# Optimization experiments

Hardware: AMD Instinct MI355X
Metric: run time of the kernel (lower is better)

Reference implementation:

```python
import jax, jax.numpy as jnp
import numpy as np

G = 4  # number of groups


def _group_vals(h, shift, Ua, Ua1, Ua2, Ua3):
    # h: [B, H]; Ua: [g, H/g, r]; Ua1/2/3: [g, r, H/g]
    B, H = h.shape
    hg = h.reshape(B, G, H // G)
    if shift:
        # torch index = rotate-left by `shift`: new group j reads old group (j+shift)%g
        hg = jnp.roll(hg, -shift, axis=1)
    t = jnp.einsum('bgd,gdr->bgr', hg, Ua)  # shared low-rank projection
    proj = lambda M: jnp.einsum('bgr,grd->bgd', t, M).reshape(B, H)
    return proj(Ua1), proj(Ua2), proj(Ua3)


def setup_inputs() -> dict:
    key = jax.random.key(0)
    ks = jax.random.split(key, 24)
    B, I, H, wR = 8192, 1024, 1024, 256
    hg = H // G
    r01, r23 = 64, 32
    d = {}
    d['x'] = jax.random.normal(ks[0], (B, I), dtype=jnp.float32)
    d['h'] = jax.random.normal(ks[1], (B, H), dtype=jnp.float32)
    d['W'] = 0.1 * jax.random.normal(ks[2], (I, wR), dtype=jnp.float32)
    d['W1'] = 0.1 * jax.random.normal(ks[3], (wR, H), dtype=jnp.float32)
    d['W2'] = 0.1 * jax.random.normal(ks[4], (wR, H), dtype=jnp.float32)
    d['W3'] = 0.1 * jax.random.normal(ks[5], (wR, H), dtype=jnp.float32)
    d['U'] = 0.1 * jax.random.normal(ks[6], (G, hg, r01), dtype=jnp.float32)
    d['U1'] = 0.1 * jax.random.normal(ks[7], (G, r01, hg), dtype=jnp.float32)
    d['U2'] = 0.1 * jax.random.normal(ks[8], (G, r01, hg), dtype=jnp.float32)
    d['U3'] = 0.1 * jax.random.normal(ks[9], (G, r01, hg), dtype=jnp.float32)
    d['UU'] = 0.1 * jax.random.normal(ks[10], (G, hg, r01), dtype=jnp.float32)
    d['UU1'] = 0.1 * jax.random.normal(ks[11], (G, r01, hg), dtype=jnp.float32)
    d['UU2'] = 0.1 * jax.random.normal(ks[12], (G, r01, hg), dtype=jnp.float32)
    d['UU3'] = 0.1 * jax.random.normal(ks[13], (G, r01, hg), dtype=jnp.float32)
    d['UUU'] = 0.1 * jax.random.normal(ks[14], (G, hg, r23), dtype=jnp.float32)
    d['UUU1'] = 0.1 * jax.random.normal(ks[15], (G, r23, hg), dtype=jnp.float32)
    d['UUU2'] = 0.1 * jax.random.normal(ks[16], (G, r23, hg), dtype=jnp.float32)
    d['UUU3'] = 0.1 * jax.random.normal(ks[17], (G, r23, hg), dtype=jnp.float32)
    d['UUUU'] = 0.1 * jax.random.normal(ks[18], (G, hg, r23), dtype=jnp.float32)
    d['UUUU1'] = 0.1 * jax.random.normal(ks[19], (G, r23, hg), dtype=jnp.float32)
    d['UUUU2'] = 0.1 * jax.random.normal(ks[20], (G, r23, hg), dtype=jnp.float32)
    d['UUUU3'] = 0.1 * jax.random.normal(ks[21], (G, r23, hg), dtype=jnp.float32)
    d['bias_r'] = jnp.ones((1, H), dtype=jnp.float32)
    d['bias_gate'] = jnp.ones((1, H), dtype=jnp.float32)
    d['bias_update'] = jnp.ones((1, H), dtype=jnp.float32)
    return d


def reference(x, h, W, W1, W2, W3, U, U1, U2, U3, UU, UU1, UU2, UU3,
              UUU, UUU1, UUU2, UUU3, UUUU, UUUU1, UUUU2, UUUU3,
              bias_r, bias_gate, bias_update):
    u1, u2, u3 = _group_vals(h, 0, U, U1, U2, U3)
    uu1, uu2, uu3 = _group_vals(h, 1, UU, UU1, UU2, UU3)
    uuu1, uuu2, uuu3 = _group_vals(h, 2, UUU, UUU1, UUU2, UUU3)
    uuuu1, uuuu2, uuuu3 = _group_vals(h, 3, UUUU, UUUU1, UUUU2, UUUU3)
    xw = x @ W  # [B, wRank]
    w1, w2, w3 = xw @ W1, xw @ W2, xw @ W3
    r = jax.nn.sigmoid(w1 + u1 + uu1 + uuu1 + uuuu1 + bias_r)
    z = jax.nn.sigmoid(w2 + u2 + uu2 + uuu2 + uuuu2 + bias_gate)
    c_tilda = jnp.tanh(w3 + r * (u3 + uu3 + uuu3 + uuuu3) + bias_update)
    return z * h + (1.0 - z) * c_tilda
```

## Files before the change

kernel.cpp:

```cpp
#include <hip/hip_runtime.h>

typedef short bf16x8 __attribute__((ext_vector_type(8)));
typedef float f32x4 __attribute__((ext_vector_type(4)));

__device__ __forceinline__ unsigned short f2bf(float f) {
  union { float f; unsigned u; } c; c.f = f;
  unsigned u = c.u;
  u += 0x7FFFu + ((u >> 16) & 1u);
  return (unsigned short)(u >> 16);
}
__device__ __forceinline__ float bf2f(unsigned short h) {
  union { unsigned u; float f; } c; c.u = ((unsigned)h) << 16;
  return c.f;
}
__device__ __forceinline__ void split2(float v, unsigned short& hi, unsigned short& lo) {
  union { float f; unsigned u; } c; c.f = v;
  unsigned uh = c.u & 0xFFFF0000u;
  hi = (unsigned short)(uh >> 16);
  union { unsigned u; float f; } d; d.u = uh;
  lo = f2bf(v - d.f);
}
__device__ __forceinline__ void gload16(const void* g, void* l) {
  __builtin_amdgcn_global_load_lds((const __attribute__((address_space(1))) void*)g,
                                   (__attribute__((address_space(3))) void*)l, 16, 0, 0);
}
__device__ __forceinline__ float sigm(float x) { return 1.0f / (1.0f + __expf(-x)); }
__device__ __forceinline__ float tanha(float x) { return 1.0f - 2.0f / (1.0f + __expf(2.0f * x)); }

__global__ __launch_bounds__(256) void s123(
    const float* __restrict__ W,
    const float* __restrict__ U, const float* __restrict__ UU,
    const float* __restrict__ UUU, const float* __restrict__ UUUU,
    const float* __restrict__ W1, const float* __restrict__ W2, const float* __restrict__ W3,
    const float* __restrict__ A1, const float* __restrict__ A2, const float* __restrict__ A3,
    const float* __restrict__ B1, const float* __restrict__ B2, const float* __restrict__ B3,
    const float* __restrict__ C1, const float* __restrict__ C2, const float* __restrict__ C3,
    const float* __restrict__ D1, const float* __restrict__ D2, const float* __restrict__ D3,
    unsigned short* __restrict__ Wt, unsigned short* __restrict__ Bg,
    unsigned short* __restrict__ Btp) {
  int gidx = blockIdx.x * 256 + threadIdx.x;
  if (gidx < 262144) {
    int idx = gidx;
    int n = idx >> 10, k = idx & 1023;
    Wt[idx] = f2bf(W[k * 256 + n]);
  } else if (gidx < 458752) {
    int idx = gidx - 262144;
    int g = idx / 49152;
    int rem = idx - g * 49152;
    int n = rem >> 8, k = rem & 255;
    int jj = 0, rr = n;
#pragma unroll
    for (int s = 0; s < 3; ++s) {
      int w = (((g - jj) & 3) < 2) ? 64 : 32;
      if (rr >= w) { rr -= w; ++jj; }
    }
    int v = (g - jj) & 3;
    int rv = (v < 2) ? 64 : 32;
    const float* M = (v == 0) ? U : (v == 1) ? UU : (v == 2) ? UUU : UUUU;
    Bg[idx] = f2bf(M[(jj * 256 + k) * rv + rr]);
  } else {
    int idx = gidx - 458752;
    int j  = idx / 540672;
    int r1 = idx - j * 540672;
    int kt = r1 / 49152;
    int r2 = r1 - kt * 49152;
    int c2 = r2 / 3072;
    int r3 = r2 - c2 * 3072;
    int q  = r3 >> 10;
    int r4 = r3 & 1023;
    int c16 = r4 >> 6;
    int k2  = r4 & 63;
    int c = c2 * 16 + c16;
    float val;
    if (kt < 8) {
      int kk = (kt * 64 + k2) & 255;
      const float* Wp = (q == 0) ? W1 : (q == 1) ? W2 : W3;
      val = Wp[kk * 1024 + j * 256 + c];
    } else {
      int kT = (kt - 8) * 64 + k2;
      int v, r, rv;
      if (kT < 64)       { v = 0; r = kT;       rv = 64; }
      else if (kT < 128) { v = 1; r = kT - 64;  rv = 64; }
      else if (kT < 160) { v = 2; r = kT - 128; rv = 32; }
      else               { v = 3; r = kT - 160; rv = 32; }
      const float* M;
      if (v == 0)      M = (q == 0) ? A1 : (q == 1) ? A2 : A3;
      else if (v == 1) M = (q == 0) ? B1 : (q == 1) ? B2 : B3;
      else if (v == 2) M = (q == 0) ? C1 : (q == 1) ? C2 : C3;
      else             M = (q == 0) ? D1 : (q == 1) ? D2 : D3;
      val = M[(j * rv + r) * 256 + c];
    }
    Btp[idx] = f2bf(val);
  }
}

__global__ __launch_bounds__(256) void g1_xw(const float* __restrict__ x,
                                             const unsigned short* __restrict__ Wt,
                                             unsigned short* __restrict__ Abuf) {
  __shared__ char lds[49152];
  const int tid = threadIdx.x, lane = tid & 63, wid = tid >> 6;
  const int mb = blockIdx.x, nb = blockIdx.y;
  const int wn = wid;
  f32x4 acc[2][2] = {};
  float4 xr[2];
  const int r0 = tid >> 4, f4c = tid & 15;
  const float* xbase = x + (size_t)(mb * 32) * 1024 + f4c * 4;

  auto loadX = [&](int kt) {
#pragma unroll
    for (int q = 0; q < 2; ++q)
      xr[q] = *(const float4*)(xbase + (size_t)(q * 16 + r0) * 1024 + kt * 64);
  };
  auto writeA = [&](int buf) {
#pragma unroll
    for (int q = 0; q < 2; ++q) {
      int row = q * 16 + r0;
      float4 v = xr[q];
      unsigned short h0, h1, h2, h3, l0, l1, l2, l3;
      split2(v.x, h0, l0); split2(v.y, h1, l1);
      split2(v.z, h2, l2); split2(v.w, h3, l3);
      int ba = row * 128 + ((f4c * 8) ^ ((row & 7) << 4));
      *(uint2*)(lds + buf * 4096 + ba) =
          make_uint2(((unsigned)h1 << 16) | h0, ((unsigned)h3 << 16) | h2);
      *(uint2*)(lds + 8192 + buf * 4096 + ba) =
          make_uint2(((unsigned)l1 << 16) | l0, ((unsigned)l3 << 16) | l2);
    }
  };
  auto stageB = [&](int kt, int buf) {
#pragma unroll
    for (int it = 0; it < 4; ++it) {
      int nloc = it * 32 + wid * 8 + (lane >> 3);
      const char* src = (const char*)Wt + (size_t)(nb * 128 + nloc) * 2048 + kt * 128
                        + (((lane & 7) * 16) ^ ((nloc & 7) << 4));
      gload16(src, lds + 16384 + buf * 16384 + (it * 32 + wid * 8) * 128);
    }
  };

  loadX(0); stageB(0, 0); writeA(0);
  __syncthreads();
#pragma unroll 2
  for (int kt = 0; kt < 16; ++kt) {
    int buf = kt & 1;
    if (kt < 15) {
      loadX(kt + 1); stageB(kt + 1, buf ^ 1);
      asm volatile("s_waitcnt vmcnt(6)" ::: "memory");
    } else {
      asm volatile("s_waitcnt vmcnt(0)" ::: "memory");
    }
    __builtin_amdgcn_s_barrier();
    __builtin_amdgcn_sched_barrier(0);
    const char* hA = lds + buf * 4096;
    const char* lA = lds + 8192 + buf * 4096;
    const char* bB = lds + 16384 + buf * 16384;
#pragma unroll
    for (int ks = 0; ks < 2; ++ks) {
      bf16x8 ah[2], al[2], b[2];
#pragma unroll
      for (int mf = 0; mf < 2; ++mf) {
        int mloc = mf * 16 + (lane & 15);
        int ka = (ks * 64 + (lane >> 4) * 16) ^ ((mloc & 7) << 4);
        ah[mf] = *(const bf16x8*)(hA + mloc * 128 + ka);
        al[mf] = *(const bf16x8*)(lA + mloc * 128 + ka);
      }
#pragma unroll
      for (int nf = 0; nf < 2; ++nf) {
        int nloc = wn * 32 + nf * 16 + (lane & 15);
        int kb = (ks * 64 + (lane >> 4) * 16) ^ ((nloc & 7) << 4);
        b[nf] = *(const bf16x8*)(bB + nloc * 128 + kb);
      }
#pragma unroll
      for (int mf = 0; mf < 2; ++mf)
#pragma unroll
        for (int nf = 0; nf < 2; ++nf) {
          acc[mf][nf] = __builtin_amdgcn_mfma_f32_16x16x32_bf16(ah[mf], b[nf], acc[mf][nf], 0, 0, 0);
          acc[mf][nf] = __builtin_amdgcn_mfma_f32_16x16x32_bf16(al[mf], b[nf], acc[mf][nf], 0, 0, 0);
        }
    }
    if (kt < 15) writeA(buf ^ 1);
    __builtin_amdgcn_sched_barrier(0);
    asm volatile("s_waitcnt lgkmcnt(0)" ::: "memory");
    __builtin_amdgcn_s_barrier();
  }
#pragma unroll
  for (int mf = 0; mf < 2; ++mf)
#pragma unroll
    for (int nf = 0; nf < 2; ++nf)
#pragma unroll
      for (int r = 0; r < 4; ++r) {
        int row = mb * 32 + mf * 16 + (lane >> 4) * 4 + r;
        int col = nb * 128 + wn * 32 + nf * 16 + (lane & 15);
        float val = acc[mf][nf][r];
        unsigned short hi, lo;
        split2(val, hi, lo);
        Abuf[(size_t)row * 1280 + col] = hi;
        Abuf[(size_t)row * 1280 + 256 + col] = lo;
      }
}

__global__ __launch_bounds__(256) void g2_t(const float* __restrict__ h,
                                            const unsigned short* __restrict__ Bg,
                                            unsigned short* __restrict__ Abuf) {
  __shared__ char lds[65536];
  const int tid = threadIdx.x, lane = tid & 63, wid = tid >> 6;
  const int mb = blockIdx.x, g = blockIdx.y;
  const int wm = wid >> 1, wn = wid & 1;
  f32x4 acc[2][6] = {};
  float4 hr[4];
  const int r0 = tid >> 4, f4c = tid & 15;
  const float* hbase = h + (size_t)(mb * 64) * 1024 + g * 256 + f4c * 4;

  auto loadH = [&](int kt) {
#pragma unroll
    for (int q = 0; q < 4; ++q)
      hr[q] = *(const float4*)(hbase + (size_t)(q * 16 + r0) * 1024 + kt * 64);
  };
  auto writeA = [&](int buf) {
#pragma unroll
    for (int q = 0; q < 4; ++q) {
      int row = q * 16 + r0;
      float4 v = hr[q];
      int ba = row * 128 + ((f4c * 8) ^ ((row & 7) << 4));
      *(uint2*)(lds + buf * 8192 + ba) =
          make_uint2(((unsigned)f2bf(v.y) << 16) | f2bf(v.x),
                     ((unsigned)f2bf(v.w) << 16) | f2bf(v.z));
    }
  };
  auto stageB = [&](int kt, int buf) {
#pragma unroll
    for (int it = 0; it < 6; ++it) {
      int nloc = it * 32 + wid * 8 + (lane >> 3);
      const char* src = (const char*)Bg + (size_t)(g * 192 + nloc) * 512 + kt * 128
                        + (((lane & 7) * 16) ^ ((nloc & 7) << 4));
      gload16(src, lds + 16384 + buf * 24576 + (it * 32 + wid * 8) * 128);
    }
  };

  loadH(0); stageB(0, 0); writeA(0);
  __syncthreads();
#pragma unroll
  for (int kt = 0; kt < 4; ++kt) {
    int buf = kt & 1;
    if (kt < 3) { loadH(kt + 1); stageB(kt + 1, buf ^ 1); }
    const char* cA = lds + buf * 8192;
    const char* cB = lds + 16384 + buf * 24576;
#pragma unroll
    for (int ks = 0; ks < 2; ++ks) {
      bf16x8 a[2], b[6];
#pragma unroll
      for (int mf = 0; mf < 2; ++mf) {
        int mloc = wm * 32 + mf * 16 + (lane & 15);
        int ka = (ks * 64 + (lane >> 4) * 16) ^ ((mloc & 7) << 4);
        a[mf] = *(const bf16x8*)(cA + mloc * 128 + ka);
      }
#pragma unroll
      for (int nf = 0; nf < 6; ++nf) {
        int nloc = wn * 96 + nf * 16 + (lane & 15);
        int kb = (ks * 64 + (lane >> 4) * 16) ^ ((nloc & 7) << 4);
        b[nf] = *(const bf16x8*)(cB + nloc * 128 + kb);
      }
#pragma unroll
      for (int mf = 0; mf < 2; ++mf)
#pragma unroll
        for (int nf = 0; nf < 6; ++nf)
          acc[mf][nf] = __builtin_amdgcn_mfma_f32_16x16x32_bf16(a[mf], b[nf], acc[mf][nf], 0, 0, 0);
    }
    if (kt < 3) writeA(buf ^ 1);
    __syncthreads();
  }
#pragma unroll
  for (int mf = 0; mf < 2; ++mf)
#pragma unroll
    for (int nf = 0; nf < 6; ++nf) {
      int n = wn * 96 + nf * 16 + (lane & 15);
      int jj = 0, rr = n;
#pragma unroll
      for (int s = 0; s < 3; ++s) {
        int w = (((g - jj) & 3) < 2) ? 64 : 32;
        if (rr >= w) { rr -= w; ++jj; }
      }
      int v = (g - jj) & 3;
      int offv = (v < 2) ? (v << 6) : (64 + (v << 5));
      int col = 512 + jj * 192 + offv + rr;
#pragma unroll
      for (int r = 0; r < 4; ++r) {
        int row = mb * 64 + wm * 32 + mf * 16 + (lane >> 4) * 4 + r;
        Abuf[(size_t)row * 1280 + col] = f2bf(acc[mf][nf][r]);
      }
    }
}

__global__ __launch_bounds__(256) void g3_main(const unsigned short* __restrict__ Abuf,
                                               const unsigned short* __restrict__ Btp,
                                               const float* __restrict__ h,
                                               const float* __restrict__ bias_r,
                                               const float* __restrict__ bias_g,
                                               const float* __restrict__ bias_u,
                                               float* __restrict__ out) {
  __shared__ char lds[57344];
  const int tid = threadIdx.x, lane = tid & 63, wid = tid >> 6;
  const int mb = blockIdx.x, nb = blockIdx.y, j = blockIdx.z;
  const int wm = wid >> 1, wn = wid & 1;
  f32x4 acc[4][4] = {};

  const char* AbufB = (const char*)Abuf + (size_t)mb * 128 * 2560;
  const char* BtpJ  = (const char*)Btp + (size_t)j * 1081344;
  int thrA[4], dstA[4], thrB[3], dstB[3];
#pragma unroll
  for (int it = 0; it < 4; ++it) {
    int mloc = wid * 32 + it * 8 + (lane >> 3);
    thrA[it] = mloc * 2560 + (((lane & 7) * 16) ^ ((mloc & 7) << 4));
    dstA[it] = wid * 4096 + it * 1024;
  }
#pragma unroll
  for (int it = 0; it < 3; ++it) {
    int row = it * 32 + wid * 8 + (lane >> 3);
    thrB[it] = row * 128 + (((lane & 7) * 16) ^ ((row & 7) << 4));
    dstB[it] = (it * 32 + wid * 8) * 128;
  }
  const char* pA[4][2];
  const char* pB[3][2];
#pragma unroll
  for (int mf = 0; mf < 4; ++mf) {
    int mloc = wm * 64 + mf * 16 + (lane & 15);
#pragma unroll
    for (int ks = 0; ks < 2; ++ks)
      pA[mf][ks] = lds + mloc * 128 + ((ks * 64 + (lane >> 4) * 16) ^ ((mloc & 7) << 4));
  }
#pragma unroll
  for (int q = 0; q < 3; ++q) {
    int nloc = wn * 48 + q * 16 + (lane & 15);
#pragma unroll
    for (int ks = 0; ks < 2; ++ks)
      pB[q][ks] = lds + 32768 + nloc * 128 + ((ks * 64 + (lane >> 4) * 16) ^ ((nloc & 7) << 4));
  }

  auto stage = [&](int kt, int buf) {
    int colb2 = (kt < 8) ? kt * 128 : (1024 + j * 384 + (kt - 8) * 128);
#pragma unroll
    for (int it = 0; it < 4; ++it)
      gload16(AbufB + colb2 + thrA[it], lds + buf * 16384 + dstA[it]);
    const char* bsrc = BtpJ + (size_t)(kt * 16 + nb * 2) * 6144;
#pragma unroll
    for (int it = 0; it < 3; ++it)
      gload16(bsrc + thrB[it], lds + 32768 + buf * 12288 + dstB[it]);
  };

  stage(0, 0);
#pragma unroll
  for (int kt = 0; kt < 11; ++kt) {
    int buf = kt & 1;
    if (kt < 10) {
      stage(kt + 1, buf ^ 1);
      asm volatile("s_waitcnt vmcnt(7)" ::: "memory");
    } else {
      asm volatile("s_waitcnt vmcnt(0)" ::: "memory");
    }
    __builtin_amdgcn_s_barrier();
    __builtin_amdgcn_sched_barrier(0);
    __builtin_amdgcn_s_setprio(1);
#pragma unroll
    for (int ks = 0; ks < 2; ++ks) {
      bf16x8 a[4];
#pragma unroll
      for (int mf = 0; mf < 4; ++mf)
        a[mf] = *(const bf16x8*)(pA[mf][ks] + buf * 16384);
#pragma unroll
      for (int q = 0; q < 3; ++q) {
        int p = (kt < 8) ? q : ((q == 2) ? 3 : q);
        bf16x8 b = *(const bf16x8*)(pB[q][ks] + buf * 12288);
#pragma unroll
        for (int mf = 0; mf < 4; ++mf)
          acc[mf][p] = __builtin_amdgcn_mfma_f32_16x16x32_bf16(a[mf], b, acc[mf][p], 0, 0, 0);
      }
    }
    __builtin_amdgcn_s_setprio(0);
    __builtin_amdgcn_sched_barrier(0);
    asm volatile("s_waitcnt lgkmcnt(0)" ::: "memory");
    __builtin_amdgcn_s_barrier();
  }
  int cg = j * 256 + nb * 32 + wn * 16 + (lane & 15);
  float br = bias_r[cg], bg = bias_g[cg], bu = bias_u[cg];
#pragma unroll
  for (int mf = 0; mf < 4; ++mf)
#pragma unroll
    for (int r = 0; r < 4; ++r) {
      int row = mb * 128 + wm * 64 + mf * 16 + (lane >> 4) * 4 + r;
      float p0 = acc[mf][0][r], p1 = acc[mf][1][r];
      float p2 = acc[mf][2][r], p3 = acc[mf][3][r];
      float rr = sigm(p0 + br);
      float zz = sigm(p1 + bg);
      float ct = tanha(p2 + rr * p3 + bu);
      float hv = h[(size_t)row * 1024 + cg];
      out[(size_t)row * 1024 + cg] = zz * hv + (1.0f - zz) * ct;
    }
}

extern "C" void kernel_launch(void* const* d_in, const int* in_sizes, int n_in,
                              void* d_out, int out_size, void* d_ws, size_t ws_size,
                              hipStream_t stream) {
  const float* x   = (const float*)d_in[0];
  const float* h   = (const float*)d_in[1];
  const float* W   = (const float*)d_in[2];
  const float* W1  = (const float*)d_in[3];
  const float* W2  = (const float*)d_in[4];
  const float* W3  = (const float*)d_in[5];
  const float* U   = (const float*)d_in[6];
  const float* U1  = (const float*)d_in[7];
  const float* U2  = (const float*)d_in[8];
  const float* U3  = (const float*)d_in[9];
  const float* UU   = (const float*)d_in[10];
  const float* UU1  = (const float*)d_in[11];
  const float* UU2  = (const float*)d_in[12];
  const float* UU3  = (const float*)d_in[13];
  const float* UUU   = (const float*)d_in[14];
  const float* UUU1  = (const float*)d_in[15];
  const float* UUU2  = (const float*)d_in[16];
  const float* UUU3  = (const float*)d_in[17];
  const float* UUUU   = (const float*)d_in[18];
  const float* UUUU1  = (const float*)d_in[19];
  const float* UUUU2  = (const float*)d_in[20];
  const float* UUUU3  = (const float*)d_in[21];
  const float* bias_r = (const float*)d_in[22];
  const float* bias_g = (const float*)d_in[23];
  const float* bias_u = (const float*)d_in[24];

  char* ws = (char*)d_ws;
  unsigned short* Abuf = (unsigned short*)(ws);
  unsigned short* Wt   = (unsigned short*)(ws + 20971520);
  unsigned short* Bg   = (unsigned short*)(ws + 21495808);
  unsigned short* Btp  = (unsigned short*)(ws + 21889024);
  float* out = (float*)d_out;

  s123<<<10240, 256, 0, stream>>>(W, U, UU, UUU, UUUU,
                                  W1, W2, W3, U1, U2, U3, UU1, UU2, UU3,
                                  UUU1, UUU2, UUU3, UUUU1, UUUU2, UUUU3,
                                  Wt, Bg, Btp);
  g1_xw<<<dim3(256, 2), 256, 0, stream>>>(x, Wt, Abuf);
  g2_t<<<dim3(128, 4), 256, 0, stream>>>(h, Bg, Abuf);
  g3_main<<<dim3(64, 8, 4), 256, 0, stream>>>(Abuf, Btp, h, bias_r, bias_g, bias_u, out);
}
```

Baseline: 97.08 us.

## Store A operand in MFMA fragment order and load it directly to registers

The producer kernels now write the intermediate A buffer in a fragment-major layout matching the MFMA 16x16x32 operand order, instead of row-major. The main GEMM loads A fragments straight from global memory into registers with double buffering, and stages only B through LDS. This drops the A staging through LDS, shrinks shared memory use and cuts LDS traffic, which may allow more blocks per CU. In exchange it costs more registers for the prefetched fragments, makes the producer writes scattered, and changes the vmcnt wait accounting.

```diff
diff --git a/kernel.cpp b/kernel.cpp
--- a/kernel.cpp
+++ b/kernel.cpp
@@ -26,6 +26,15 @@
 }
 __device__ __forceinline__ float sigm(float x) { return 1.0f / (1.0f + __expf(-x)); }
 __device__ __forceinline__ float tanha(float x) { return 1.0f - 2.0f / (1.0f + __expf(2.0f * x)); }
+
+__device__ __forceinline__ int fragIdx(int row, int col) {
+  int rowblk = row >> 4;
+  int cc = col >> 6;
+  int ks = (col >> 5) & 1;
+  int ln = (((col >> 3) & 3) << 4) | (row & 15);
+  int e = col & 7;
+  return (((rowblk * 20 + cc) * 2 + ks) << 9) + ln * 8 + e;
+}
 
 __global__ __launch_bounds__(256) void s123(
     const float* __restrict__ W,
@@ -192,8 +201,8 @@
         float val = acc[mf][nf][r];
         unsigned short hi, lo;
         split2(val, hi, lo);
-        Abuf[(size_t)row * 1280 + col] = hi;
-        Abuf[(size_t)row * 1280 + 256 + col] = lo;
+        Abuf[fragIdx(row, col)] = hi;
+        Abuf[fragIdx(row, col + 256)] = lo;
       }
 }
 
@@ -284,7 +293,7 @@
 #pragma unroll
       for (int r = 0; r < 4; ++r) {
         int row = mb * 64 + wm * 32 + mf * 16 + (lane >> 4) * 4 + r;
-        Abuf[(size_t)row * 1280 + col] = f2bf(acc[mf][nf][r]);
+        Abuf[fragIdx(row, col)] = f2bf(acc[mf][nf][r]);
       }
     }
 }
@@ -296,62 +305,61 @@
                                                const float* __restrict__ bias_g,
                                                const float* __restrict__ bias_u,
                                                float* __restrict__ out) {
-  __shared__ char lds[57344];
+  __shared__ char lds[24576];
   const int tid = threadIdx.x, lane = tid & 63, wid = tid >> 6;
   const int mb = blockIdx.x, nb = blockIdx.y, j = blockIdx.z;
   const int wm = wid >> 1, wn = wid & 1;
   f32x4 acc[4][4] = {};
 
-  const char* AbufB = (const char*)Abuf + (size_t)mb * 128 * 2560;
+  const char* AbufB = (const char*)Abuf + (size_t)(mb * 8 + wm * 4) * 40960 + lane * 16;
   const char* BtpJ  = (const char*)Btp + (size_t)j * 1081344;
-  int thrA[4], dstA[4], thrB[3], dstB[3];
-#pragma unroll
-  for (int it = 0; it < 4; ++it) {
-    int mloc = wid * 32 + it * 8 + (lane >> 3);
-    thrA[it] = mloc * 2560 + (((lane & 7) * 16) ^ ((mloc & 7) << 4));
-    dstA[it] = wid * 4096 + it * 1024;
-  }
+  int thrB[3], dstB[3];
 #pragma unroll
   for (int it = 0; it < 3; ++it) {
     int row = it * 32 + wid * 8 + (lane >> 3);
     thrB[it] = row * 128 + (((lane & 7) * 16) ^ ((row & 7) << 4));
     dstB[it] = (it * 32 + wid * 8) * 128;
   }
-  const char* pA[4][2];
   const char* pB[3][2];
-#pragma unroll
-  for (int mf = 0; mf < 4; ++mf) {
-    int mloc = wm * 64 + mf * 16 + (lane & 15);
-#pragma unroll
-    for (int ks = 0; ks < 2; ++ks)
-      pA[mf][ks] = lds + mloc * 128 + ((ks * 64 + (lane >> 4) * 16) ^ ((mloc & 7) << 4));
-  }
 #pragma unroll
   for (int q = 0; q < 3; ++q) {
     int nloc = wn * 48 + q * 16 + (lane & 15);
 #pragma unroll
     for (int ks = 0; ks < 2; ++ks)
-      pB[q][ks] = lds + 32768 + nloc * 128 + ((ks * 64 + (lane >> 4) * 16) ^ ((nloc & 7) << 4));
-  }
-
-  auto stage = [&](int kt, int buf) {
-    int colb2 = (kt < 8) ? kt * 128 : (1024 + j * 384 + (kt - 8) * 128);
-#pragma unroll
-    for (int it = 0; it < 4; ++it)
-      gload16(AbufB + colb2 + thrA[it], lds + buf * 16384 + dstA[it]);
+      pB[q][ks] = lds + nloc * 128 + ((ks * 64 + (lane >> 4) * 16) ^ ((nloc & 7) << 4));
+  }
+
+  auto stageB = [&](int kt, int buf) {
     const char* bsrc = BtpJ + (size_t)(kt * 16 + nb * 2) * 6144;
 #pragma unroll
     for (int it = 0; it < 3; ++it)
-      gload16(bsrc + thrB[it], lds + 32768 + buf * 12288 + dstB[it]);
-  };
-
-  stage(0, 0);
+      gload16(bsrc + thrB[it], lds + buf * 12288 + dstB[it]);
+  };
+  bf16x8 aF[2][8];
+  auto loadA = [&](int kt, int slot) {
+    int cc = (kt < 8) ? kt : (8 + j * 3 + (kt - 8));
+#pragma unroll
+    for (int mf = 0; mf < 4; ++mf)
+#pragma unroll
+      for (int ks = 0; ks < 2; ++ks)
+        aF[slot][mf * 2 + ks] =
+            *(const bf16x8*)(AbufB + (size_t)mf * 40960 + cc * 2048 + ks * 1024);
+  };
+
+  stageB(0, 0);
+  __builtin_amdgcn_sched_barrier(0);
+  loadA(0, 0);
+  __builtin_amdgcn_sched_barrier(0);
+
 #pragma unroll
   for (int kt = 0; kt < 11; ++kt) {
-    int buf = kt & 1;
+    const int cur = kt & 1;
     if (kt < 10) {
-      stage(kt + 1, buf ^ 1);
-      asm volatile("s_waitcnt vmcnt(7)" ::: "memory");
+      stageB(kt + 1, cur ^ 1);
+      __builtin_amdgcn_sched_barrier(0);
+      loadA(kt + 1, cur ^ 1);
+      __builtin_amdgcn_sched_barrier(0);
+      asm volatile("s_waitcnt vmcnt(11)" ::: "memory");
     } else {
       asm volatile("s_waitcnt vmcnt(0)" ::: "memory");
     }
@@ -360,17 +368,14 @@
     __builtin_amdgcn_s_setprio(1);
 #pragma unroll
     for (int ks = 0; ks < 2; ++ks) {
-      bf16x8 a[4];
-#pragma unroll
-      for (int mf = 0; mf < 4; ++mf)
-        a[mf] = *(const bf16x8*)(pA[mf][ks] + buf * 16384);
 #pragma unroll
       for (int q = 0; q < 3; ++q) {
         int p = (kt < 8) ? q : ((q == 2) ? 3 : q);
-        bf16x8 b = *(const bf16x8*)(pB[q][ks] + buf * 12288);
+        bf16x8 b = *(const bf16x8*)(pB[q][ks] + cur * 12288);
 #pragma unroll
         for (int mf = 0; mf < 4; ++mf)
-          acc[mf][p] = __builtin_amdgcn_mfma_f32_16x16x32_bf16(a[mf], b, acc[mf][p], 0, 0, 0);
+          acc[mf][p] = __builtin_amdgcn_mfma_f32_16x16x32_bf16(aF[cur][mf * 2 + ks], b,
+                                                               acc[mf][p], 0, 0, 0);
       }
     }
     __builtin_amdgcn_s_setprio(0);
```

New measurement: 103.7 us. 6.8% more time.

## Double the N tile of the final gated GEMM to reuse A tiles

Applied to the files above, without the earlier changes.

The final fused GEMM+gate kernel now covers 64 output columns per block instead of 32. Each wave computes two column fragments per gate, so every A fragment loaded from LDS feeds twice as many MFMAs, and the grid is halved in y. The aim is to cut redundant A-tile global and LDS traffic. In exchange the block uses more LDS and twice the accumulator registers, which can lower occupancy, and the grid shrinks to 1024 blocks.

```diff
diff --git a/kernel.cpp b/kernel.cpp
--- a/kernel.cpp
+++ b/kernel.cpp
@@ -296,62 +296,63 @@
                                                const float* __restrict__ bias_g,
                                                const float* __restrict__ bias_u,
                                                float* __restrict__ out) {
-  __shared__ char lds[57344];
+  __shared__ char lds[81920];
   const int tid = threadIdx.x, lane = tid & 63, wid = tid >> 6;
-  const int mb = blockIdx.x, nb = blockIdx.y, j = blockIdx.z;
+  const int mb = blockIdx.x, cb = blockIdx.y, j = blockIdx.z;
   const int wm = wid >> 1, wn = wid & 1;
-  f32x4 acc[4][4] = {};
+  f32x4 acc[4][8] = {};
 
   const char* AbufB = (const char*)Abuf + (size_t)mb * 128 * 2560;
   const char* BtpJ  = (const char*)Btp + (size_t)j * 1081344;
-  int thrA[4], dstA[4], thrB[3], dstB[3];
+  int thrA[4], dstA[4], thrB[6], dstB[6];
 #pragma unroll
   for (int it = 0; it < 4; ++it) {
     int mloc = wid * 32 + it * 8 + (lane >> 3);
     thrA[it] = mloc * 2560 + (((lane & 7) * 16) ^ ((mloc & 7) << 4));
-    dstA[it] = wid * 4096 + it * 1024;
-  }
-#pragma unroll
-  for (int it = 0; it < 3; ++it) {
-    int row = it * 32 + wid * 8 + (lane >> 3);
-    thrB[it] = row * 128 + (((lane & 7) * 16) ^ ((row & 7) << 4));
+    dstA[it] = (wid * 32 + it * 8) * 128;
+  }
+#pragma unroll
+  for (int it = 0; it < 6; ++it) {
+    int rB = it * 32 + wid * 8 + (lane >> 3);
+    thrB[it] = rB * 128 + (((lane & 7) * 16) ^ ((rB & 7) << 4));
     dstB[it] = (it * 32 + wid * 8) * 128;
   }
-  const char* pA[4][2];
-  const char* pB[3][2];
+  int pA[4][2], pB[3][2][2];
 #pragma unroll
   for (int mf = 0; mf < 4; ++mf) {
     int mloc = wm * 64 + mf * 16 + (lane & 15);
 #pragma unroll
     for (int ks = 0; ks < 2; ++ks)
-      pA[mf][ks] = lds + mloc * 128 + ((ks * 64 + (lane >> 4) * 16) ^ ((mloc & 7) << 4));
-  }
-#pragma unroll
-  for (int q = 0; q < 3; ++q) {
-    int nloc = wn * 48 + q * 16 + (lane & 15);
-#pragma unroll
-    for (int ks = 0; ks < 2; ++ks)
-      pB[q][ks] = lds + 32768 + nloc * 128 + ((ks * 64 + (lane >> 4) * 16) ^ ((nloc & 7) << 4));
-  }
+      pA[mf][ks] = mloc * 128 + ((ks * 64 + (lane >> 4) * 16) ^ ((mloc & 7) << 4));
+  }
+#pragma unroll
+  for (int q = 0; q < 3; ++q)
+#pragma unroll
+    for (int cf = 0; cf < 2; ++cf) {
+      int rB = ((wn * 2 + cf) * 3 + q) * 16 + (lane & 15);
+#pragma unroll
+      for (int ks = 0; ks < 2; ++ks)
+        pB[q][cf][ks] = 32768 + rB * 128 + ((ks * 64 + (lane >> 4) * 16) ^ ((rB & 7) << 4));
+    }
 
   auto stage = [&](int kt, int buf) {
     int colb2 = (kt < 8) ? kt * 128 : (1024 + j * 384 + (kt - 8) * 128);
 #pragma unroll
     for (int it = 0; it < 4; ++it)
       gload16(AbufB + colb2 + thrA[it], lds + buf * 16384 + dstA[it]);
-    const char* bsrc = BtpJ + (size_t)(kt * 16 + nb * 2) * 6144;
-#pragma unroll
-    for (int it = 0; it < 3; ++it)
-      gload16(bsrc + thrB[it], lds + 32768 + buf * 12288 + dstB[it]);
+    const char* bsrc = BtpJ + (size_t)(kt * 16 + cb * 4) * 6144;
+#pragma unroll
+    for (int it = 0; it < 6; ++it)
+      gload16(bsrc + thrB[it], lds + buf * 24576 + 32768 + dstB[it]);
   };
 
   stage(0, 0);
 #pragma unroll
   for (int kt = 0; kt < 11; ++kt) {
-    int buf = kt & 1;
+    const int buf = kt & 1;
     if (kt < 10) {
       stage(kt + 1, buf ^ 1);
-      asm volatile("s_waitcnt vmcnt(7)" ::: "memory");
+      asm volatile("s_waitcnt vmcnt(10)" ::: "memory");
     } else {
       asm volatile("s_waitcnt vmcnt(0)" ::: "memory");
     }
@@ -363,14 +364,18 @@
       bf16x8 a[4];
 #pragma unroll
       for (int mf = 0; mf < 4; ++mf)
-        a[mf] = *(const bf16x8*)(pA[mf][ks] + buf * 16384);
+        a[mf] = *(const bf16x8*)(lds + buf * 16384 + pA[mf][ks]);
 #pragma unroll
       for (int q = 0; q < 3; ++q) {
-        int p = (kt < 8) ? q : ((q == 2) ? 3 : q);
-        bf16x8 b = *(const bf16x8*)(pB[q][ks] + buf * 12288);
-#pragma unroll
-        for (int mf = 0; mf < 4; ++mf)
-          acc[mf][p] = __builtin_amdgcn_mfma_f32_16x16x32_bf16(a[mf], b, acc[mf][p], 0, 0, 0);
+        const int p = (kt < 8) ? q : ((q == 2) ? 3 : q);
+#pragma unroll
+        for (int cf = 0; cf < 2; ++cf) {
+          bf16x8 b = *(const bf16x8*)(lds + buf * 24576 + pB[q][cf][ks]);
+#pragma unroll
+          for (int mf = 0; mf < 4; ++mf)
+            acc[mf][p * 2 + cf] =
+                __builtin_amdgcn_mfma_f32_16x16x32_bf16(a[mf], b, acc[mf][p * 2 + cf], 0, 0, 0);
+        }
       }
     }
     __builtin_amdgcn_s_setprio(0);
@@ -378,21 +383,24 @@
     asm volatile("s_waitcnt lgkmcnt(0)" ::: "memory");
     __builtin_amdgcn_s_barrier();
   }
-  int cg = j * 256 + nb * 32 + wn * 16 + (lane & 15);
-  float br = bias_r[cg], bg = bias_g[cg], bu = bias_u[cg];
-#pragma unroll
-  for (int mf = 0; mf < 4; ++mf)
-#pragma unroll
-    for (int r = 0; r < 4; ++r) {
-      int row = mb * 128 + wm * 64 + mf * 16 + (lane >> 4) * 4 + r;
-      float p0 = acc[mf][0][r], p1 = acc[mf][1][r];
-      float p2 = acc[mf][2][r], p3 = acc[mf][3][r];
-      float rr = sigm(p0 + br);
-      float zz = sigm(p1 + bg);
-      float ct = tanha(p2 + rr * p3 + bu);
-      float hv = h[(size_t)row * 1024 + cg];
-      out[(size_t)row * 1024 + cg] = zz * hv + (1.0f - zz) * ct;
-    }
+#pragma unroll
+  for (int cf = 0; cf < 2; ++cf) {
+    int cg = j * 256 + cb * 64 + wn * 32 + cf * 16 + (lane & 15);
+    float br = bias_r[cg], bg = bias_g[cg], bu = bias_u[cg];
+#pragma unroll
+    for (int mf = 0; mf < 4; ++mf)
+#pragma unroll
+      for (int r = 0; r < 4; ++r) {
+        int row = mb * 128 + wm * 64 + mf * 16 + (lane >> 4) * 4 + r;
+        float p0 = acc[mf][0 + cf][r], p1 = acc[mf][2 + cf][r];
+        float p2 = acc[mf][4 + cf][r], p3 = acc[mf][6 + cf][r];
+        float rr = sigm(p0 + br);
+        float zz = sigm(p1 + bg);
+        float ct = tanha(p2 + rr * p3 + bu);
+        float hv = h[(size_t)row * 1024 + cg];
+        out[(size_t)row * 1024 + cg] = zz * hv + (1.0f - zz) * ct;
+      }
+  }
 }
 
 extern "C" void kernel_launch(void* const* d_in, const int* in_sizes, int n_in,
@@ -437,5 +445,5 @@
                                   Wt, Bg, Btp);
   g1_xw<<<dim3(256, 2), 256, 0, stream>>>(x, Wt, Abuf);
   g2_t<<<dim3(128, 4), 256, 0, stream>>>(h, Bg, Abuf);
-  g3_main<<<dim3(64, 8, 4), 256, 0, stream>>>(Abuf, Btp, h, bias_r, bias_g, bias_u, out);
-}
+  g3_main<<<dim3(64, 4, 4), 256, 0, stream>>>(Abuf, Btp, h, bias_r, bias_g, bias_u, out);
+}
```

Result: faster. 93.03 us (-4.2%).
